# Optimization experiments

Hardware: AMD Instinct MI355X
Metric: run time of the kernel (lower is better)

The kernel has to match this reference:

```python
import jax, jax.numpy as jnp
import numpy as np

B, C_IN, T, N_VERTEX = 2, 64, 12, 2048
KS, C_OUT = 3, 64
NNZ = 98304  # Ks * n_vertex * avg_degree(16)


def setup_inputs() -> dict:
    key = jax.random.key(0)
    k0, k1, k2, k3, k4, k5 = jax.random.split(key, 6)
    x = jax.random.normal(k0, (B, C_IN, T, N_VERTEX), jnp.float32)
    # kaiming-uniform-ish init for weight [Ks, c_in, c_out]
    bound_w = float(np.sqrt(6.0 / C_IN))
    weight = jax.random.uniform(k1, (KS, C_IN, C_OUT), jnp.float32, -bound_w, bound_w)
    bound_b = float(1.0 / np.sqrt(C_OUT))
    bias = jax.random.uniform(k2, (C_OUT,), jnp.float32, -bound_b, bound_b)
    # sparse chebconv_filter in COO: shape [n_vertex, Ks*n_vertex]
    filter_rows = jax.random.randint(k3, (NNZ,), 0, N_VERTEX)
    filter_cols = jax.random.randint(k4, (NNZ,), 0, KS * N_VERTEX)
    filter_vals = jax.random.normal(k5, (NNZ,), jnp.float32) * 0.1
    return dict(x=x, weight=weight, bias=bias, filter_vals=filter_vals,
                filter_rows=filter_rows, filter_cols=filter_cols)


def reference(x, weight, bias, filter_vals, filter_rows, filter_cols):
    b, c_in, t, n = x.shape
    ks, _, c_out = weight.shape
    # dense GEMM: [B*T*n (row-major flatten of B,c_in,T,n keeping last dim c_in), c_in] @ [c_in, Ks*c_out]
    xw = x.reshape(-1, c_in) @ weight.reshape(c_in, ks * c_out)  # [B*c_in*T*n/c_in, Ks*c_out]
    xw = xw.reshape(n * ks, -1)                                  # [n*Ks, B*T*c_out]
    # spmm with COO filter [n, n*Ks]: gather columns, scale, scatter-add to rows
    gathered = filter_vals[:, None] * xw[filter_cols]            # [nnz, B*T*c_out]
    y = jax.ops.segment_sum(gathered, filter_rows, num_segments=N_VERTEX)  # [n, B*T*c_out]
    return y.reshape(-1, c_out) + bias                           # [n*B*T, c_out]
```

## Files before the change

### kernel.cpp

```cpp
#include <hip/hip_runtime.h>
#include <hip/hip_bf16.h>

#define NV      2048
#define NNZ_    98304
#define KDIM    64
#define WCOLS   192
#define ZROWS   16384
#define BUCKET  128

typedef __attribute__((ext_vector_type(8))) short  short8;
typedef __attribute__((ext_vector_type(8))) unsigned short ushort8;
typedef __attribute__((ext_vector_type(4))) float  float4v;

__device__ __forceinline__ float b2f(unsigned short h) {
    return __uint_as_float(((unsigned int)h) << 16);
}
__device__ __forceinline__ unsigned short f2b(float f) {
    return __bfloat16_as_ushort(__float2bfloat16(f));
}

__global__ __launch_bounds__(256) void scatter_kernel(
    const int4* __restrict__ rows4, const int4* __restrict__ cols4,
    const float4* __restrict__ vals4, const float* __restrict__ wf,
    int* __restrict__ cnt, int2* __restrict__ sedge,
    unsigned short* __restrict__ wt)
{
    if (blockIdx.x == NNZ_ / 1024) {
        for (int i = 0; i < 48; i++) {
            const int e = threadIdx.x + 256 * i;
            const int k = e / WCOLS, n = e - k * WCOLS;
            wt[n * KDIM + k] = f2b(wf[e]);
        }
        return;
    }
    const int t = blockIdx.x * 256 + threadIdx.x;
    const int4   r = rows4[t];
    const int4   c = cols4[t];
    const float4 v = vals4[t];
    int p;
    p = atomicAdd(&cnt[r.x], 1); if (p < BUCKET) sedge[r.x * BUCKET + p] = make_int2(c.x * 512, __float_as_int(v.x));
    p = atomicAdd(&cnt[r.y], 1); if (p < BUCKET) sedge[r.y * BUCKET + p] = make_int2(c.y * 512, __float_as_int(v.y));
    p = atomicAdd(&cnt[r.z], 1); if (p < BUCKET) sedge[r.z * BUCKET + p] = make_int2(c.z * 512, __float_as_int(v.z));
    p = atomicAdd(&cnt[r.w], 1); if (p < BUCKET) sedge[r.w * BUCKET + p] = make_int2(c.w * 512, __float_as_int(v.w));
}

__global__ __launch_bounds__(64) void spmmx_kernel(
    const float* __restrict__ xf,
    const int* __restrict__ cnt,
    const int2* __restrict__ sedge,
    unsigned short* __restrict__ zb)
{
    const int b    = blockIdx.x;
    const int g    = b & 7;
    const int row  = b >> 3;
    const int lane = threadIdx.x;

    int n = cnt[row];
    if (n > BUCKET) n = BUCKET;
    const int2* se = sedge + row * BUCKET;
    const int off = g * KDIM + lane;

    float acc = 0.f;
    int i = 0;
    for (; i + 4 <= n; i += 4) {
        const int2 e0 = se[i], e1 = se[i + 1], e2 = se[i + 2], e3 = se[i + 3];
        const float x0 = xf[e0.x + off];
        const float x1 = xf[e1.x + off];
        const float x2 = xf[e2.x + off];
        const float x3 = xf[e3.x + off];
        acc += __int_as_float(e0.y) * x0 + __int_as_float(e1.y) * x1
             + __int_as_float(e2.y) * x2 + __int_as_float(e3.y) * x3;
    }
    for (; i < n; i++) {
        const int2 e = se[i];
        acc += __int_as_float(e.y) * xf[e.x + off];
    }
    zb[(size_t)(row * 8 + g) * KDIM + lane] = f2b(acc);
}

__global__ __launch_bounds__(256) void gemm2_kernel(
    const unsigned short* __restrict__ zb, const unsigned short* __restrict__ wt,
    const float* __restrict__ bias, float* __restrict__ out)
{
    __shared__ unsigned short Wt[WCOLS * 72];
    __shared__ unsigned short Zs[64 * 72];
    const int tid = threadIdx.x;
    const int m0  = blockIdx.x * 64;

#pragma unroll
    for (int u = 0; u < 2; u++) {
        const int ch = tid + 256 * u;
        const ushort8 p = *(const ushort8*)(zb + (size_t)m0 * KDIM + ch * 8);
        const int row = ch >> 3, col = (ch & 7) * 8;
        *(ushort8*)&Zs[row * 72 + col] = p;
    }
#pragma unroll
    for (int u = 0; u < 6; u++) {
        const int ch = tid + 256 * u;
        const ushort8 p = *(const ushort8*)(wt + ch * 8);
        const int row = ch >> 3, col = (ch & 7) * 8;
        *(ushort8*)&Wt[row * 72 + col] = p;
    }
    __syncthreads();

    const int lane = tid & 63;
    const int mt   = tid >> 6;
    const int q    = lane >> 4;
    const int c    = lane & 15;

    const short8 a0 = *(const short8*)&Zs[(mt * 16 + c) * 72 + q * 8];
    const short8 a1 = *(const short8*)&Zs[(mt * 16 + c) * 72 + 32 + q * 8];

    float4v acc[12];
#pragma unroll
    for (int nt = 0; nt < 12; nt++) {
        const short8 b0 = *(const short8*)&Wt[(nt * 16 + c) * 72 + q * 8];
        const short8 b1 = *(const short8*)&Wt[(nt * 16 + c) * 72 + 32 + q * 8];
        float4v d = {0.f, 0.f, 0.f, 0.f};
        d = __builtin_amdgcn_mfma_f32_16x16x32_bf16(a0, b0, d, 0, 0, 0);
        d = __builtin_amdgcn_mfma_f32_16x16x32_bf16(a1, b1, d, 0, 0, 0);
        acc[nt] = d;
    }

    const int rbase = m0 + mt * 16 + q * 4;
#pragma unroll
    for (int nt = 0; nt < 12; nt++) {
        const int col = nt * 16 + c;
        const float bb = bias[col & 63];
#pragma unroll
        for (int r = 0; r < 4; r++)
            out[(size_t)(rbase + r) * WCOLS + col] = acc[nt][r] + bb;
    }
}

extern "C" void kernel_launch(void* const* d_in, const int* in_sizes, int n_in,
                              void* d_out, int out_size, void* d_ws, size_t ws_size,
                              hipStream_t stream) {
    const float* x    = (const float*)d_in[0];
    const float* wgt  = (const float*)d_in[1];
    const float* bias = (const float*)d_in[2];
    const float* fval = (const float*)d_in[3];
    const int* frow   = (const int*)d_in[4];
    const int* fcol   = (const int*)d_in[5];

    int* cnt = (int*)d_ws;
    int2* sedge = (int2*)(cnt + 2048);
    unsigned short* wt = (unsigned short*)(sedge + NV * BUCKET);
    unsigned short* zb = wt + 12288;

    hipMemsetAsync(cnt, 0, 2048 * sizeof(int), stream);
    scatter_kernel<<<NNZ_ / 1024 + 1, 256, 0, stream>>>(
        (const int4*)frow, (const int4*)fcol, (const float4*)fval, wgt,
        cnt, sedge, wt);
    spmmx_kernel <<<NV * 8,    64,  0, stream>>>(x, cnt, sedge, zb);
    gemm2_kernel <<<ZROWS / 64, 256, 0, stream>>>(zb, wt, bias, (float*)d_out);
}
```

Measured before the change: 109.6 us.

## Pre-convert x to bf16 and gather bf16 in SpMM with wider edge loads

Adds x-to-bf16 conversion blocks to the scatter kernel, so the SpMM gather reads half as many bytes per neighbour. The SpMM kernel now packs four rows per 256-thread block and reads edges as int4 pairs, unrolled by eight. This cuts gather bandwidth and per-block launch overhead. In exchange it adds an extra full pass over x (read fp32, write bf16) and rounds x before accumulation, which loses precision.

```diff
diff --git a/kernel.cpp b/kernel.cpp
--- a/kernel.cpp
+++ b/kernel.cpp
@@ -7,6 +7,7 @@
 #define WCOLS   192
 #define ZROWS   16384
 #define BUCKET  128
+#define XCONV_BLKS 768
 
 typedef __attribute__((ext_vector_type(8))) short  short8;
 typedef __attribute__((ext_vector_type(8))) unsigned short ushort8;
@@ -22,10 +23,25 @@
 __global__ __launch_bounds__(256) void scatter_kernel(
     const int4* __restrict__ rows4, const int4* __restrict__ cols4,
     const float4* __restrict__ vals4, const float* __restrict__ wf,
+    const float4* __restrict__ x4,
     int* __restrict__ cnt, int2* __restrict__ sedge,
-    unsigned short* __restrict__ wt)
+    unsigned short* __restrict__ wt, unsigned short* __restrict__ xh)
 {
-    if (blockIdx.x == NNZ_ / 1024) {
+    const int b = blockIdx.x;
+    if (b < XCONV_BLKS) {
+        const int base = (b * 256 + threadIdx.x) * 4;
+        const float4 v0 = x4[base], v1 = x4[base + 1];
+        const float4 v2 = x4[base + 2], v3 = x4[base + 3];
+        ushort8 p0, p1;
+        p0[0]=f2b(v0.x); p0[1]=f2b(v0.y); p0[2]=f2b(v0.z); p0[3]=f2b(v0.w);
+        p0[4]=f2b(v1.x); p0[5]=f2b(v1.y); p0[6]=f2b(v1.z); p0[7]=f2b(v1.w);
+        p1[0]=f2b(v2.x); p1[1]=f2b(v2.y); p1[2]=f2b(v2.z); p1[3]=f2b(v2.w);
+        p1[4]=f2b(v3.x); p1[5]=f2b(v3.y); p1[6]=f2b(v3.z); p1[7]=f2b(v3.w);
+        *(ushort8*)(xh + base * 4)     = p0;
+        *(ushort8*)(xh + base * 4 + 8) = p1;
+        return;
+    }
+    if (b == XCONV_BLKS + NNZ_ / 1024) {
         for (int i = 0; i < 48; i++) {
             const int e = threadIdx.x + 256 * i;
             const int k = e / WCOLS, n = e - k * WCOLS;
@@ -33,7 +49,7 @@
         }
         return;
     }
-    const int t = blockIdx.x * 256 + threadIdx.x;
+    const int t = (b - XCONV_BLKS) * 256 + threadIdx.x;
     const int4   r = rows4[t];
     const int4   c = cols4[t];
     const float4 v = vals4[t];
@@ -44,36 +60,42 @@
     p = atomicAdd(&cnt[r.w], 1); if (p < BUCKET) sedge[r.w * BUCKET + p] = make_int2(c.w * 512, __float_as_int(v.w));
 }
 
-__global__ __launch_bounds__(64) void spmmx_kernel(
-    const float* __restrict__ xf,
+__global__ __launch_bounds__(256) void spmmx_kernel(
+    const unsigned short* __restrict__ xh,
     const int* __restrict__ cnt,
     const int2* __restrict__ sedge,
     unsigned short* __restrict__ zb)
 {
     const int b    = blockIdx.x;
     const int g    = b & 7;
-    const int row  = b >> 3;
-    const int lane = threadIdx.x;
+    const int row  = (b >> 3) * 4 + (threadIdx.x >> 6);
+    const int lane = threadIdx.x & 63;
 
     int n = cnt[row];
     if (n > BUCKET) n = BUCKET;
-    const int2* se = sedge + row * BUCKET;
+    const int4* se2 = (const int4*)(sedge + row * BUCKET);
     const int off = g * KDIM + lane;
 
     float acc = 0.f;
     int i = 0;
-    for (; i + 4 <= n; i += 4) {
-        const int2 e0 = se[i], e1 = se[i + 1], e2 = se[i + 2], e3 = se[i + 3];
-        const float x0 = xf[e0.x + off];
-        const float x1 = xf[e1.x + off];
-        const float x2 = xf[e2.x + off];
-        const float x3 = xf[e3.x + off];
-        acc += __int_as_float(e0.y) * x0 + __int_as_float(e1.y) * x1
-             + __int_as_float(e2.y) * x2 + __int_as_float(e3.y) * x3;
+    for (; i + 8 <= n; i += 8) {
+        const int4 ea = se2[(i >> 1)    ];
+        const int4 eb = se2[(i >> 1) + 1];
+        const int4 ec = se2[(i >> 1) + 2];
+        const int4 ed = se2[(i >> 1) + 3];
+        const float x0 = b2f(xh[ea.x + off]), x1 = b2f(xh[ea.z + off]);
+        const float x2 = b2f(xh[eb.x + off]), x3 = b2f(xh[eb.z + off]);
+        const float x4v = b2f(xh[ec.x + off]), x5 = b2f(xh[ec.z + off]);
+        const float x6 = b2f(xh[ed.x + off]), x7 = b2f(xh[ed.z + off]);
+        acc += __int_as_float(ea.y) * x0 + __int_as_float(ea.w) * x1
+             + __int_as_float(eb.y) * x2 + __int_as_float(eb.w) * x3
+             + __int_as_float(ec.y) * x4v + __int_as_float(ec.w) * x5
+             + __int_as_float(ed.y) * x6 + __int_as_float(ed.w) * x7;
     }
+    const int2* se = (const int2*)se2;
     for (; i < n; i++) {
         const int2 e = se[i];
-        acc += __int_as_float(e.y) * xf[e.x + off];
+        acc += __int_as_float(e.y) * b2f(xh[e.x + off]);
     }
     zb[(size_t)(row * 8 + g) * KDIM + lane] = f2b(acc);
 }
@@ -147,11 +169,12 @@
     int2* sedge = (int2*)(cnt + 2048);
     unsigned short* wt = (unsigned short*)(sedge + NV * BUCKET);
     unsigned short* zb = wt + 12288;
+    unsigned short* xh = zb + (size_t)ZROWS * KDIM;
 
     hipMemsetAsync(cnt, 0, 2048 * sizeof(int), stream);
-    scatter_kernel<<<NNZ_ / 1024 + 1, 256, 0, stream>>>(
+    scatter_kernel<<<XCONV_BLKS + NNZ_ / 1024 + 1, 256, 0, stream>>>(
         (const int4*)frow, (const int4*)fcol, (const float4*)fval, wgt,
-        cnt, sedge, wt);
-    spmmx_kernel <<<NV * 8,    64,  0, stream>>>(x, cnt, sedge, zb);
+        (const float4*)x, cnt, sedge, wt, xh);
+    spmmx_kernel <<<ZROWS / 4, 256, 0, stream>>>(xh, cnt, sedge, zb);
     gemm2_kernel <<<ZROWS / 64, 256, 0, stream>>>(zb, wt, bias, (float*)d_out);
 }
```

After: 119.7 us. 9.3% more time.
